# Performance work log

Hardware: AMD Instinct MI355X
Metric: run time of the kernel (lower is better)

## Reference

```python
import jax, jax.numpy as jnp
import numpy as np

BIT_DEPTH = 8  # feature squeezing

def setup_inputs() -> dict:
    key = jax.random.key(0)
    ks = jax.random.split(key, 8)
    B, C, H, W = 8, 256, 64, 64
    Cq = C // 8
    x = jax.random.normal(ks[0], (B, C, H, W), dtype=jnp.float32)
    # 1x1 conv weights stored as [out, in] (kernel dims squeezed)
    wq = jax.random.normal(ks[1], (Cq, C), dtype=jnp.float32) * 0.05
    bq = jax.random.normal(ks[2], (Cq,), dtype=jnp.float32) * 0.05
    wk = jax.random.normal(ks[3], (Cq, C), dtype=jnp.float32) * 0.05
    bk = jax.random.normal(ks[4], (Cq,), dtype=jnp.float32) * 0.05
    wv = jax.random.normal(ks[5], (C, C), dtype=jnp.float32) * 0.05
    bv = jax.random.normal(ks[6], (C,), dtype=jnp.float32) * 0.05
    gamma = jax.random.normal(ks[7], (1,), dtype=jnp.float32) * 0.1
    return {"x": x, "wq": wq, "bq": bq, "wk": wk, "bk": bk, "wv": wv, "bv": bv, "gamma": gamma}

def reference(x, wq, bq, wk, bk, wv, bv, gamma):
    B, C, H, W = x.shape
    N = H * W
    xf = x.reshape(B, C, N)  # flatten spatial
    # 1x1 convs == per-pixel linear projections
    q = jnp.einsum('bcn,oc->bon', xf, wq) + bq[None, :, None]   # [B, C/8, N]
    k = jnp.einsum('bcn,oc->bon', xf, wk) + bk[None, :, None]   # [B, C/8, N]
    v = jnp.einsum('bcn,oc->bon', xf, wv) + bv[None, :, None]   # [B, C, N]
    energy = jnp.einsum('bcn,bcm->bnm', q, k)                   # [B, N, N] (no scaling, as in source)
    attn = jax.nn.softmax(energy, axis=-1)
    out = jnp.einsum('bcm,bnm->bcn', v, attn).reshape(B, C, H, W)
    out = gamma[0] * out + out               # gamma-scaled residual of attention output
    scale = jnp.float32(2 ** BIT_DEPTH)
    return jnp.floor(out * scale) / scale    # feature squeezing (bit_depth=8)
```

## Files before the change

kernel.cpp:

```cpp
#include <hip/hip_runtime.h>
#include <math.h>

namespace {
constexpr int BB = 8;
constexpr int CH = 256;
constexpr int CQ = 32;
constexpr int NN = 4096;
}

typedef float f32x4 __attribute__((ext_vector_type(4)));
typedef short bf16x8 __attribute__((ext_vector_type(8)));
typedef unsigned short us8 __attribute__((ext_vector_type(8)));

#define MFMA16(a, b, c) __builtin_amdgcn_mfma_f32_16x16x32_bf16(a, b, c, 0, 0, 0)

__device__ __forceinline__ unsigned short f2bf(float x) {
    unsigned int u = __float_as_uint(x);
    u += 0x7fffu + ((u >> 16) & 1u);
    return (unsigned short)(u >> 16);
}
__device__ __forceinline__ float bf2f(unsigned short h) {
    return __uint_as_float(((unsigned int)h) << 16);
}
__device__ __forceinline__ void gload16(const void* g, void* l) {
    __builtin_amdgcn_global_load_lds(
        (const __attribute__((address_space(1))) unsigned int*)g,
        (__attribute__((address_space(3))) unsigned int*)l, 16, 0, 0);
}

__global__ __launch_bounds__(256) void wsplit_kernel(
    const float* __restrict__ wq, const float* __restrict__ wk,
    const float* __restrict__ wv,
    unsigned short* __restrict__ wh, unsigned short* __restrict__ wl)
{
    int idx = blockIdx.x * 256 + threadIdx.x;
    float v;
    if (idx < 8192)       v = wq[idx];
    else if (idx < 16384) v = wk[idx - 8192];
    else                  v = wv[idx - 16384];
    unsigned short hi = f2bf(v);
    wh[idx] = hi;
    wl[idx] = f2bf(v - bf2f(hi));
}

__global__ __launch_bounds__(256) void transpose_kernel(
    const float* __restrict__ x,
    unsigned short* __restrict__ xh, unsigned short* __restrict__ xl)
{
    __shared__ float xf[64 * 68];
    __shared__ unsigned short hs[64 * 80];
    __shared__ unsigned short ls[64 * 80];
    const int t  = threadIdx.x;
    const int b  = blockIdx.x >> 8;
    const int tl = blockIdx.x & 255;
    const int c0 = (tl >> 6) * 64;
    const int n0 = (tl & 63) * 64;

    #pragma unroll
    for (int i = 0; i < 4; ++i) {
        int idx = i * 256 + t;
        int c = idx >> 4, nf = idx & 15;
        float4 v4 = *(const float4*)(x + ((size_t)(b * 256 + c0 + c)) * NN + n0 + nf * 4);
        *(float4*)(xf + c * 68 + nf * 4) = v4;
    }
    __syncthreads();

    const int n = t & 63;
    #pragma unroll
    for (int loop = 0; loop < 2; ++loop) {
        int chunk = (t >> 6) + 4 * loop;
        us8 h8, l8;
        #pragma unroll
        for (int j = 0; j < 8; ++j) {
            float v = xf[(chunk * 8 + j) * 68 + n];
            unsigned short hi = f2bf(v);
            h8[j] = hi;
            l8[j] = f2bf(v - bf2f(hi));
        }
        *(us8*)(hs + n * 80 + chunk * 8) = h8;
        *(us8*)(ls + n * 80 + chunk * 8) = l8;
    }
    __syncthreads();

    {
        int rn = t >> 2, piece = t & 3;
        size_t grow = ((size_t)(b * NN + n0 + rn)) * 256 + c0 + piece * 16;
        *(us8*)(xh + grow)     = *(const us8*)(hs + rn * 80 + piece * 16);
        *(us8*)(xh + grow + 8) = *(const us8*)(hs + rn * 80 + piece * 16 + 8);
        *(us8*)(xl + grow)     = *(const us8*)(ls + rn * 80 + piece * 16);
        *(us8*)(xl + grow + 8) = *(const us8*)(ls + rn * 80 + piece * 16 + 8);
    }
}

#define PJ_XL 32768
#define PJ_VE 16384
__global__ __launch_bounds__(256, 2) void proj_kernel(
    const unsigned short* __restrict__ xh, const unsigned short* __restrict__ xl,
    const unsigned short* __restrict__ wh, const unsigned short* __restrict__ wl,
    const float* __restrict__ bq, const float* __restrict__ bk,
    const float* __restrict__ bv,
    unsigned short* __restrict__ qh, unsigned short* __restrict__ ql,
    unsigned short* __restrict__ kh, unsigned short* __restrict__ kl,
    unsigned short* __restrict__ vt)
{
    __shared__ __align__(16) unsigned char smem[65536];
    const int t    = threadIdx.x;
    const int lane = t & 63;
    const int w    = t >> 6;
    const int l16  = lane & 15;
    const int quad = lane >> 4;
    const int b    = blockIdx.x >> 6;
    const int n0   = (blockIdx.x & 63) << 6;

    const unsigned char* xhB = (const unsigned char*)(xh + ((size_t)b * NN + n0) * 256);
    const unsigned char* xlB = (const unsigned char*)(xl + ((size_t)b * NN + n0) * 256);
    #pragma unroll
    for (int j = 0; j < 8; ++j) {
        int idx = j * 256 + t;
        int r = idx >> 5, cl = idx & 31;
        int cg = cl ^ (r & 7);
        gload16(xhB + (size_t)r * 512 + cg * 16, smem + idx * 16);
        gload16(xlB + (size_t)r * 512 + cg * 16, smem + PJ_XL + idx * 16);
    }
    __syncthreads();

    f32x4 acc[5][4] = {};
    #pragma unroll 1
    for (int kc = 0; kc < 8; ++kc) {
        bf16x8 ah[5], al[5];
        #pragma unroll
        for (int i = 0; i < 5; ++i) {
            int och = (w * 5 + i) * 16 + l16;
            ah[i] = *(const bf16x8*)(wh + och * 256 + kc * 32 + quad * 8);
            al[i] = *(const bf16x8*)(wl + och * 256 + kc * 32 + quad * 8);
        }
        #pragma unroll
        for (int nt = 0; nt < 4; ++nt) {
            int roff = (nt * 16 + l16) * 512 + (((kc * 4 + quad) ^ (l16 & 7)) * 16);
            bf16x8 bh = *(const bf16x8*)(smem + roff);
            bf16x8 bl = *(const bf16x8*)(smem + PJ_XL + roff);
            #pragma unroll
            for (int i = 0; i < 5; ++i) {
                acc[i][nt] = MFMA16(ah[i], bh, acc[i][nt]);
                acc[i][nt] = MFMA16(al[i], bh, acc[i][nt]);
                acc[i][nt] = MFMA16(ah[i], bl, acc[i][nt]);
            }
        }
    }
    __syncthreads();

    #pragma unroll
    for (int i = 0; i < 5; ++i) {
        int tile = w * 5 + i;
        if (tile < 4) {
            #pragma unroll
            for (int r = 0; r < 4; ++r) {
                int och = tile * 16 + quad * 4 + r;
                float bias = (och < 32) ? bq[och] : bk[och - 32];
                int arr = (och < 32) ? 0 : 2;
                int oq = och & 31;
                #pragma unroll
                for (int nt = 0; nt < 4; ++nt) {
                    float val = acc[i][nt][r] + bias;
                    unsigned short hi = f2bf(val);
                    unsigned short lo = f2bf(val - bf2f(hi));
                    *(unsigned short*)(smem + arr * 4096 + (nt * 16 + l16) * 64 + oq * 2) = hi;
                    *(unsigned short*)(smem + (arr + 1) * 4096 + (nt * 16 + l16) * 64 + oq * 2) = lo;
                }
            }
        } else {
            #pragma unroll
            for (int r = 0; r < 4; ++r) {
                int voch = tile * 16 + quad * 4 + r - 64;
                float bias = bv[voch];
                #pragma unroll
                for (int nt = 0; nt < 4; ++nt) {
                    *(unsigned short*)(smem + PJ_VE + voch * 136 + (nt * 16 + l16) * 2)
                        = f2bf(acc[i][nt][r] + bias);
                }
            }
        }
    }
    __syncthreads();

    {
        unsigned short* dsts[4] = { qh, ql, kh, kl };
        int arr = t >> 6, n = t & 63;
        unsigned short* dst = dsts[arr] + ((size_t)b * NN + n0 + n) * 32;
        #pragma unroll
        for (int i = 0; i < 4; ++i)
            *(us8*)(dst + i * 8) = *(const us8*)(smem + arr * 4096 + n * 64 + i * 16);
    }
    #pragma unroll
    for (int p = 0; p < 4; ++p) {
        int voch = p * 64 + (t >> 2), piece = t & 3;
        unsigned short* dst = vt + ((size_t)b * CH + voch) * NN + n0 + piece * 16;
        *(us8*)(dst)     = *(const us8*)(smem + PJ_VE + voch * 136 + piece * 32);
        *(us8*)(dst + 8) = *(const us8*)(smem + PJ_VE + voch * 136 + piece * 32 + 16);
    }
}

#define A_P0 0
#define A_P1 9216
#define A_SM 18432

__global__ __launch_bounds__(256, 2) void attn_kernel(
    const unsigned short* __restrict__ qh, const unsigned short* __restrict__ ql,
    const unsigned short* __restrict__ kh, const unsigned short* __restrict__ kl,
    const unsigned short* __restrict__ vt, const float* __restrict__ gptr,
    float* __restrict__ out)
{
    __shared__ __align__(16) unsigned char smem[19456];
    const int t    = threadIdx.x;
    const int lane = t & 63;
    const int w    = t >> 6;
    const int l16  = lane & 15;
    const int quad = lane >> 4;
    const int b    = blockIdx.x & 7;
    const int n0   = (blockIdx.x >> 3) << 6;

    bf16x8 qhA[4], qlA[4];
    #pragma unroll
    for (int qt = 0; qt < 4; ++qt) {
        size_t row = (size_t)b * NN + n0 + qt * 16 + l16;
        qhA[qt] = *(const bf16x8*)(qh + row * 32 + quad * 8);
        qlA[qt] = *(const bf16x8*)(ql + row * 32 + quad * 8);
    }

    const unsigned short* vbase[4];
    #pragma unroll
    for (int ct = 0; ct < 4; ++ct)
        vbase[ct] = vt + (size_t)b * CH * NN
                       + (size_t)(w * 64 + ct * 16 + l16) * NN + quad * 8;
    const unsigned short* khbase = kh + ((size_t)b * NN + w * 16 + l16) * 32 + quad * 8;
    const unsigned short* klbase = kl + ((size_t)b * NN + w * 16 + l16) * 32 + quad * 8;

    f32x4 acc[4][4] = {};
    float S[4][4] = {};

    bf16x8 kch = *(const bf16x8*)(khbase);
    bf16x8 kcl = *(const bf16x8*)(klbase);

    #pragma unroll 1
    for (int tile = 0; tile < 64; ++tile) {
        const int m0 = tile * 64;
        const int m1 = ((tile + 1) & 63) * 64;

        bf16x8 vr0[4], vr1[4];
        #pragma unroll
        for (int ct = 0; ct < 4; ++ct) {
            vr0[ct] = *(const bf16x8*)(vbase[ct] + m0);
            vr1[ct] = *(const bf16x8*)(vbase[ct] + m0 + 32);
        }
        bf16x8 knh = *(const bf16x8*)(khbase + (size_t)m1 * 32);
        bf16x8 knl = *(const bf16x8*)(klbase + (size_t)m1 * 32);

        unsigned char* P = smem + ((tile & 1) ? A_P1 : A_P0);
        #pragma unroll
        for (int qt = 0; qt < 4; ++qt) {
            f32x4 e = { 0.f, 0.f, 0.f, 0.f };
            e = MFMA16(qhA[qt], kch, e);
            e = MFMA16(qlA[qt], kch, e);
            e = MFMA16(qhA[qt], kcl, e);
            #pragma unroll
            for (int r = 0; r < 4; ++r) {
                float p = __expf(e[r]);
                unsigned short pb = f2bf(p);
                S[qt][r] += bf2f(pb);
                *(unsigned short*)(P + (qt * 16 + quad * 4 + r) * 144
                                     + (w * 16 + l16) * 2) = pb;
            }
        }
        __syncthreads();

        #pragma unroll
        for (int ks = 0; ks < 2; ++ks) {
            bf16x8 af[4];
            #pragma unroll
            for (int qt = 0; qt < 4; ++qt)
                af[qt] = *(const bf16x8*)(P + (qt * 16 + l16) * 144
                                            + ks * 64 + quad * 16);
            #pragma unroll
            for (int qt = 0; qt < 4; ++qt) {
                #pragma unroll
                for (int ct = 0; ct < 4; ++ct)
                    acc[qt][ct] = MFMA16(af[qt], ks ? vr1[ct] : vr0[ct],
                                         acc[qt][ct]);
            }
        }
        kch = knh;
        kcl = knl;
    }

    #pragma unroll
    for (int mask = 1; mask <= 8; mask <<= 1)
        #pragma unroll
        for (int qt = 0; qt < 4; ++qt)
            #pragma unroll
            for (int r = 0; r < 4; ++r)
                S[qt][r] += __shfl_xor(S[qt][r], mask);
    float* SM = (float*)(smem + A_SM);
    if (l16 == 0) {
        #pragma unroll
        for (int qt = 0; qt < 4; ++qt)
            #pragma unroll
            for (int r = 0; r < 4; ++r)
                SM[w * 64 + qt * 16 + quad * 4 + r] = S[qt][r];
    }
    __syncthreads();

    const float g1 = 1.f + gptr[0];
    float* ob = out + (size_t)b * CH * NN;
    #pragma unroll
    for (int qt = 0; qt < 4; ++qt) {
        float is[4];
        #pragma unroll
        for (int r = 0; r < 4; ++r) {
            int qi = qt * 16 + quad * 4 + r;
            float Sf = SM[qi] + SM[64 + qi] + SM[128 + qi] + SM[192 + qi];
            is[r] = g1 / Sf;
        }
        #pragma unroll
        for (int ct = 0; ct < 4; ++ct) {
            float4 o4;
            o4.x = floorf(acc[qt][ct][0] * is[0] * 256.f) * 0.00390625f;
            o4.y = floorf(acc[qt][ct][1] * is[1] * 256.f) * 0.00390625f;
            o4.z = floorf(acc[qt][ct][2] * is[2] * 256.f) * 0.00390625f;
            o4.w = floorf(acc[qt][ct][3] * is[3] * 256.f) * 0.00390625f;
            *(float4*)(ob + (size_t)(w * 64 + ct * 16 + l16) * NN
                          + n0 + qt * 16 + quad * 4) = o4;
        }
    }
}

extern "C" void kernel_launch(void* const* d_in, const int* in_sizes, int n_in,
                              void* d_out, int out_size, void* d_ws, size_t ws_size,
                              hipStream_t stream) {
    const float* x  = (const float*)d_in[0];
    const float* wq = (const float*)d_in[1];
    const float* bq = (const float*)d_in[2];
    const float* wk = (const float*)d_in[3];
    const float* bk = (const float*)d_in[4];
    const float* wv = (const float*)d_in[5];
    const float* bv = (const float*)d_in[6];
    const float* gm = (const float*)d_in[7];
    float* out = (float*)d_out;

    unsigned short* ws = (unsigned short*)d_ws;
    const size_t XSZ = (size_t)BB * NN * 256;
    const size_t WSZ = 320 * 256;
    const size_t QSZ = (size_t)BB * NN * 32;
    unsigned short* xh = ws;
    unsigned short* xl = xh + XSZ;
    unsigned short* wh = xl + XSZ;
    unsigned short* wl = wh + WSZ;
    unsigned short* qh = wl + WSZ;
    unsigned short* ql = qh + QSZ;
    unsigned short* kh = ql + QSZ;
    unsigned short* kl = kh + QSZ;
    unsigned short* vt = kl + QSZ;

    wsplit_kernel<<<320, 256, 0, stream>>>(wq, wk, wv, wh, wl);
    transpose_kernel<<<2048, 256, 0, stream>>>(x, xh, xl);
    proj_kernel<<<512, 256, 0, stream>>>(xh, xl, wh, wl, bq, bk, bv,
                                         qh, ql, kh, kl, vt);
    attn_kernel<<<512, 256, 0, stream>>>(qh, ql, kh, kl, vt, gm, out);
}
```

Before: 268.8 us.

## Stage V tiles through double-buffered swizzled LDS with async global loads

Each V tile is now copied into a double-buffered LDS region with 16-byte global-to-LDS loads, issued one tile ahead, instead of every wave reading its V fragments straight from global memory inside the loop. The P buffer and the V buffer both use an XOR swizzle to avoid LDS bank conflicts, and the MFMA block is wrapped in s_setprio. The aim is to hide and coalesce V memory traffic behind compute. In exchange, shared memory grows to 80 KB per block, which puts pressure on the two-blocks-per-CU occupancy target, and the final reduction area now overlaps the first V buffer.

```diff
diff --git a/kernel.cpp b/kernel.cpp
--- a/kernel.cpp
+++ b/kernel.cpp
@@ -201,8 +201,10 @@
 }
 
 #define A_P0 0
-#define A_P1 9216
-#define A_SM 18432
+#define A_P1 8192
+#define A_V0 16384
+#define A_V1 49152
+#define A_SM 16384
 
 __global__ __launch_bounds__(256, 2) void attn_kernel(
     const unsigned short* __restrict__ qh, const unsigned short* __restrict__ ql,
@@ -210,7 +212,7 @@
     const unsigned short* __restrict__ vt, const float* __restrict__ gptr,
     float* __restrict__ out)
 {
-    __shared__ __align__(16) unsigned char smem[19456];
+    __shared__ __align__(16) unsigned char smem[81920];
     const int t    = threadIdx.x;
     const int lane = t & 63;
     const int w    = t >> 6;
@@ -227,35 +229,27 @@
         qlA[qt] = *(const bf16x8*)(ql + row * 32 + quad * 8);
     }
 
-    const unsigned short* vbase[4];
-    #pragma unroll
-    for (int ct = 0; ct < 4; ++ct)
-        vbase[ct] = vt + (size_t)b * CH * NN
-                       + (size_t)(w * 64 + ct * 16 + l16) * NN + quad * 8;
     const unsigned short* khbase = kh + ((size_t)b * NN + w * 16 + l16) * 32 + quad * 8;
     const unsigned short* klbase = kl + ((size_t)b * NN + w * 16 + l16) * 32 + quad * 8;
+    const unsigned char*  vtB    = (const unsigned char*)(vt + (size_t)b * CH * NN);
 
     f32x4 acc[4][4] = {};
     float S[4][4] = {};
 
     bf16x8 kch = *(const bf16x8*)(khbase);
     bf16x8 kcl = *(const bf16x8*)(klbase);
+    #pragma unroll
+    for (int j = 0; j < 8; ++j) {
+        int idx = j * 256 + t;
+        int r = idx >> 3, cl = idx & 7;
+        int cg = cl ^ (r & 7);
+        gload16(vtB + (size_t)r * 8192 + cg * 16, smem + A_V0 + idx * 16);
+    }
 
     #pragma unroll 1
     for (int tile = 0; tile < 64; ++tile) {
-        const int m0 = tile * 64;
-        const int m1 = ((tile + 1) & 63) * 64;
-
-        bf16x8 vr0[4], vr1[4];
-        #pragma unroll
-        for (int ct = 0; ct < 4; ++ct) {
-            vr0[ct] = *(const bf16x8*)(vbase[ct] + m0);
-            vr1[ct] = *(const bf16x8*)(vbase[ct] + m0 + 32);
-        }
-        bf16x8 knh = *(const bf16x8*)(khbase + (size_t)m1 * 32);
-        bf16x8 knl = *(const bf16x8*)(klbase + (size_t)m1 * 32);
-
         unsigned char* P = smem + ((tile & 1) ? A_P1 : A_P0);
+        const int key = w * 16 + l16;
         #pragma unroll
         for (int qt = 0; qt < 4; ++qt) {
             f32x4 e = { 0.f, 0.f, 0.f, 0.f };
@@ -267,26 +261,53 @@
                 float p = __expf(e[r]);
                 unsigned short pb = f2bf(p);
                 S[qt][r] += bf2f(pb);
-                *(unsigned short*)(P + (qt * 16 + quad * 4 + r) * 144
-                                     + (w * 16 + l16) * 2) = pb;
-            }
-        }
+                int row = qt * 16 + quad * 4 + r;
+                *(unsigned short*)(P + row * 128
+                                     + ((((key >> 3) ^ (row & 7)) << 4)
+                                        | ((key & 7) << 1))) = pb;
+            }
+        }
+
         __syncthreads();
 
+        const int m1 = ((tile + 1) & 63) * 64;
+        bf16x8 knh = *(const bf16x8*)(khbase + (size_t)m1 * 32);
+        bf16x8 knl = *(const bf16x8*)(klbase + (size_t)m1 * 32);
+        if (tile < 63) {
+            unsigned char* vdst = smem + ((tile & 1) ? A_V0 : A_V1);
+            const unsigned char* vsrc = vtB + (size_t)m1 * 2;
+            #pragma unroll
+            for (int j = 0; j < 8; ++j) {
+                int idx = j * 256 + t;
+                int r = idx >> 3, cl = idx & 7;
+                int cg = cl ^ (r & 7);
+                gload16(vsrc + (size_t)r * 8192 + cg * 16, vdst + idx * 16);
+            }
+        }
+
+        const unsigned char* VB = smem + ((tile & 1) ? A_V1 : A_V0);
         #pragma unroll
         for (int ks = 0; ks < 2; ++ks) {
-            bf16x8 af[4];
+            bf16x8 af[4], bfr[4];
+            #pragma unroll
+            for (int qt = 0; qt < 4; ++qt) {
+                int row = qt * 16 + l16;
+                af[qt] = *(const bf16x8*)(P + row * 128
+                                            + (((ks * 4 + quad) ^ (row & 7)) << 4));
+            }
+            #pragma unroll
+            for (int ct = 0; ct < 4; ++ct) {
+                int vrow = w * 64 + ct * 16 + l16;
+                int ch = (ks * 4 + quad) ^ (l16 & 7);
+                bfr[ct] = *(const bf16x8*)(VB + vrow * 128 + ch * 16);
+            }
+            __builtin_amdgcn_s_setprio(1);
             #pragma unroll
             for (int qt = 0; qt < 4; ++qt)
-                af[qt] = *(const bf16x8*)(P + (qt * 16 + l16) * 144
-                                            + ks * 64 + quad * 16);
-            #pragma unroll
-            for (int qt = 0; qt < 4; ++qt) {
                 #pragma unroll
                 for (int ct = 0; ct < 4; ++ct)
-                    acc[qt][ct] = MFMA16(af[qt], ks ? vr1[ct] : vr0[ct],
-                                         acc[qt][ct]);
-            }
+                    acc[qt][ct] = MFMA16(af[qt], bfr[ct], acc[qt][ct]);
+            __builtin_amdgcn_s_setprio(0);
         }
         kch = knh;
         kcl = knl;
```

New measurement: 246.2 us. 1.09x faster.
